# Kernel optimization log

Measured on AMD Instinct MI355X. Metric: run time of the kernel, lower is better.

## Reference

```python
import jax, jax.numpy as jnp
import numpy as np
from jax import lax

LEAK = 0.2
SCALE = 2.0 ** 0.5

def _make_blur_kernel(upsample_factor=1):
    k1 = jnp.array([1.0, 3.0, 3.0, 1.0], dtype=jnp.float32)
    k = k1[None, :] * k1[:, None]
    k = k / jnp.sum(k)
    return k * (upsample_factor ** 2)

def _modulate(weight, s):
    # weight [O,I,k,k], s [B,I] -> [B,O,I,k,k], demodulated
    wm = s[:, None, :, None, None] * weight[None]
    d = lax.rsqrt(jnp.sum(wm * wm, axis=(2, 3, 4)) + 1e-8)  # [B,O]
    return d[:, :, None, None, None] * wm

def _conv_transpose_sample(xi, wi):
    # xi [I,H,W], wi [O,I,k,k] (already ordered as wm[o,i]); torch conv_transpose2d(stride=2, pad=0)
    k = wi.shape[-1]
    y = lax.conv_general_dilated(xi[None], jnp.flip(wi, (-2, -1)), (1, 1),
                                 [(k - 1, k - 1), (k - 1, k - 1)], lhs_dilation=(2, 2),
                                 dimension_numbers=('NCHW', 'OIHW', 'NCHW'))
    return y[0]

def _conv_same_sample(xi, wi):
    y = lax.conv_general_dilated(xi[None], wi, (1, 1), [(1, 1), (1, 1)],
                                 dimension_numbers=('NCHW', 'OIHW', 'NCHW'))
    return y[0]

def _blur(x, kern, pad):
    # upfirdn2d with up=1, down=1, pad=(pad,pad): depthwise correlate with flipped kernel
    C = x.shape[1]
    w = jnp.tile(jnp.flip(kern, (0, 1))[None, None], (C, 1, 1, 1))
    return lax.conv_general_dilated(x, w, (1, 1), [(pad, pad), (pad, pad)],
                                    feature_group_count=C,
                                    dimension_numbers=('NCHW', 'OIHW', 'NCHW'))

def _flrelu(x, b):
    y = x + b.reshape(1, -1, 1, 1)
    return jnp.where(y >= 0, y, LEAK * y) * SCALE

def setup_inputs() -> dict:
    key = jax.random.key(0)
    ks = jax.random.split(key, 15)
    B, Cin, Cout, L, H = 8, 512, 256, 512, 64
    return {
        'x': jax.random.normal(ks[0], (B, Cin, H, H), jnp.float32),
        'w1': jax.random.normal(ks[1], (B, L), jnp.float32),
        'w2': jax.random.normal(ks[2], (B, L), jnp.float32),
        'noise1': jax.random.normal(ks[3], (B, 1, 2 * H, 2 * H), jnp.float32),
        'noise2': jax.random.normal(ks[4], (B, 1, 2 * H, 2 * H), jnp.float32),
        'weight1': jax.random.normal(ks[5], (Cout, Cin, 3, 3), jnp.float32) * 0.1,
        'aff1_w': jax.random.normal(ks[6], (Cin, L), jnp.float32) * 0.04,
        'aff1_b': jax.random.normal(ks[7], (Cin,), jnp.float32) * 0.1,
        'weight2': jax.random.normal(ks[8], (Cout, Cout, 3, 3), jnp.float32) * 0.1,
        'aff2_w': jax.random.normal(ks[9], (Cout, L), jnp.float32) * 0.04,
        'aff2_b': jax.random.normal(ks[10], (Cout,), jnp.float32) * 0.1,
        'ns1': jax.random.normal(ks[11], (1, 1, 1, 1), jnp.float32) * 0.1,
        'ns2': jax.random.normal(ks[12], (1, 1, 1, 1), jnp.float32) * 0.1,
        'b1': jax.random.normal(ks[13], (Cout,), jnp.float32) * 0.1,
        'b2': jax.random.normal(ks[14], (Cout,), jnp.float32) * 0.1,
    }

def reference(x, w1, w2, noise1, noise2, weight1, aff1_w, aff1_b,
              weight2, aff2_w, aff2_b, ns1, ns2, b1, b2):
    # conv1: modulated conv_transpose (upsample), blur, noise, fused leaky relu
    s1 = w1 @ aff1_w.T + aff1_b + 1.0          # [B, Cin]
    wm1 = _modulate(weight1, s1)               # [B, O, I, 3, 3]
    y = jax.vmap(_conv_transpose_sample)(x, wm1)  # [B, O, 129, 129]
    y = _blur(y, _make_blur_kernel(2), 1)      # [B, O, 128, 128]
    y = y + ns1 * noise1
    y = _flrelu(y, b1)
    # conv2: modulated same-padding conv, noise, fused leaky relu
    s2 = w2 @ aff2_w.T + aff2_b + 1.0
    wm2 = _modulate(weight2, s2)
    y = jax.vmap(_conv_same_sample)(y, wm2)
    y = y + ns2 * noise2
    y = _flrelu(y, b2)
    return y
```

## Files before the change

kernel.cpp:

```cpp
#include <hip/hip_runtime.h>
#include <hip/hip_bf16.h>

#define SQRT2C 1.41421356237309515f
#define LEAKF 0.2f

typedef __attribute__((ext_vector_type(4))) float f32x4;
typedef __attribute__((ext_vector_type(8))) __bf16 bf16x8;
typedef unsigned int u32x4 __attribute__((ext_vector_type(4)));

#define GLOAD16(g, l) \
  __builtin_amdgcn_global_load_lds((const __attribute__((address_space(1))) void*)(const void*)(g), \
                                   (__attribute__((address_space(3))) void*)(void*)(l), 16, 0, 0)

__device__ __forceinline__ unsigned short f2bf(float f) {
  unsigned int u = __float_as_uint(f);
  unsigned int r = (u + 0x7fffu + ((u >> 16) & 1u)) >> 16;
  return (unsigned short)r;
}
__device__ __forceinline__ float bflo(unsigned int w) { return __uint_as_float(w << 16); }
__device__ __forceinline__ float bfhi(unsigned int w) { return __uint_as_float(w & 0xffff0000u); }

constexpr float B1v(int c) { return (c < 0 || c > 3) ? 0.f : ((c == 0 || c == 3) ? 1.f : 3.f); }

__global__ void k_affine(const float* __restrict__ w, const float* __restrict__ aw,
                         const float* __restrict__ ab, float* __restrict__ s, int C) {
  int wid = (blockIdx.x * blockDim.x + threadIdx.x) >> 6;
  int lane = threadIdx.x & 63;
  int b = wid / C, i = wid % C;
  const float* wr = w + (size_t)b * 512;
  const float* ar = aw + (size_t)i * 512;
  float acc = 0.f;
  #pragma unroll
  for (int l = 0; l < 512; l += 64) acc += wr[l + lane] * ar[l + lane];
  #pragma unroll
  for (int off = 32; off; off >>= 1) acc += __shfl_down(acc, off, 64);
  if (lane == 0) s[wid] = acc + ab[i] + 1.0f;
}

__global__ void k_demod(const float* __restrict__ weight, const float* __restrict__ s,
                        float* __restrict__ d, int CIN) {
  int o = blockIdx.x & 255, b = blockIdx.x >> 8;
  int t = threadIdx.x;
  const float* wr = weight + (size_t)o * CIN * 9;
  const float* sr = s + (size_t)b * CIN;
  float acc = 0.f;
  for (int i = t; i < CIN; i += 256) {
    float sv = sr[i];
    float ws = 0.f;
    #pragma unroll
    for (int k = 0; k < 9; ++k) { float w = wr[(size_t)i * 9 + k]; ws += w * w; }
    acc += sv * sv * ws;
  }
  __shared__ float red[256];
  red[t] = acc; __syncthreads();
  for (int h = 128; h; h >>= 1) { if (t < h) red[t] += red[t + h]; __syncthreads(); }
  if (t == 0) d[blockIdx.x] = rsqrtf(red[0] + 1e-8f);
}

__global__ void k_wvert(const float* __restrict__ w1, const float* __restrict__ s1,
                        const float* __restrict__ d1, unsigned short* __restrict__ Wv) {
  int t = blockIdx.x * 256 + threadIdx.x;
  int i = t & 511, o = (t >> 9) & 255, b = t >> 17;
  float sd = s1[b * 512 + i] * d1[b * 256 + o];
  const float* wp = w1 + ((size_t)o * 512 + i) * 9;
  float wm[3][3];
  #pragma unroll
  for (int ky = 0; ky < 3; ++ky)
    #pragma unroll
    for (int kx = 0; kx < 3; ++kx) wm[ky][kx] = wp[ky * 3 + kx] * sd;
  #pragma unroll
  for (int rp = 0; rp < 2; ++rp)
    #pragma unroll
    for (int u = 0; u < 3; ++u)
      #pragma unroll
      for (int kx = 0; kx < 3; ++kx) {
        float v = 0.f;
        #pragma unroll
        for (int ky = 0; ky < 3; ++ky) v += B1v(4 - 2 * u - ky + rp) * wm[ky][kx];
        Wv[(((size_t)(b * 6 + rp * 3 + kx)) * 3 + u) * 131072 + (size_t)o * 512 + i] = f2bf(v);
      }
}

__global__ void k_weff2(const float* __restrict__ w2, const float* __restrict__ s2,
                        const float* __restrict__ d2, unsigned short* __restrict__ Wm) {
  int t = blockIdx.x * 256 + threadIdx.x;
  int i = t & 255, o = (t >> 8) & 255, b = t >> 16;
  float sd = s2[b * 256 + i] * d2[b * 256 + o];
  const float* wp = w2 + ((size_t)o * 256 + i) * 9;
  #pragma unroll
  for (int k = 0; k < 9; ++k)
    Wm[((size_t)(b * 9 + k) * 256 + o) * 256 + i] = f2bf(wp[k] * sd);
}

__global__ void k_border_y1(unsigned short* __restrict__ y1p) {
  int t = blockIdx.x * 256 + threadIdx.x;
  int l = t & 31;
  int c = (t >> 5) % 516;
  int b = (t >> 5) / 516;
  int p_, q_;
  if (c < 130)      { p_ = 0;       q_ = c; }
  else if (c < 260) { p_ = 129;     q_ = c - 130; }
  else if (c < 388) { p_ = c - 259; q_ = 0; }
  else              { p_ = c - 387; q_ = 129; }
  uint4* p = (uint4*)(y1p + (((size_t)(b * 130) + p_) * 130 + q_) * 256);
  p[l] = make_uint4(0u, 0u, 0u, 0u);
}

__global__ void k_fillv(unsigned short* __restrict__ xt) {
  int t = blockIdx.x * 256 + threadIdx.x;
  int j = t & 4095;
  int r = (t >> 12) & 1;
  int b = t >> 13;
  uint4* p = (uint4*)(xt + ((size_t)(b * 66) + (r ? 65 : 0)) * 64 * 512);
  p[j] = make_uint4(0u, 0u, 0u, 0u);
}

__global__ void k_txpose(const float* __restrict__ x, unsigned short* __restrict__ xt) {
  int bid = blockIdx.x;
  int i0 = (bid & 7) * 64;
  int x0 = ((bid >> 3) & 1) * 32;
  int y  = (bid >> 4) & 63;
  int b  = bid >> 10;
  int tx = threadIdx.x & 31, ty = threadIdx.x >> 5;
  __shared__ float tile[64][33];
  const float* xp = x + ((size_t)(b * 512 + i0) * 64 + y) * 64 + x0;
  for (int ii = ty; ii < 64; ii += 8) tile[ii][tx] = xp[(size_t)ii * 4096 + tx];
  __syncthreads();
  unsigned short* op = xt + (((size_t)(b * 66) + y + 1) * 64 + x0) * 512 + i0;
  for (int xx = ty; xx < 32; xx += 8) {
    int iL = tx * 2;
    unsigned int pk = (unsigned int)f2bf(tile[iL][xx]) | ((unsigned int)f2bf(tile[iL + 1][xx]) << 16);
    *(unsigned int*)&op[(size_t)xx * 512 + iL] = pk;
  }
}

template<int CIN, int GSH, int HP, int RHO_N, int TAPS, int PANB, int OM>
__global__ __launch_bounds__(512, 2) void k_conv8(
    const unsigned short* __restrict__ Xt,
    const unsigned short* __restrict__ Wt,
    const float* __restrict__ noise,
    const float* __restrict__ nsp,
    const float* __restrict__ bias,
    unsigned short* __restrict__ Yb,
    float* __restrict__ Yf)
{
  constexpr int GRID = 1 << GSH;
  constexpr int NT = (GRID * GRID) / 256;
  constexpr int NKT = TAPS * (CIN / 32);
  constexpr int KMASK = (CIN / 32) - 1;
  constexpr int KSH = (CIN == 512) ? 4 : 3;
  constexpr int TOT = NT * RHO_N * 8;
  constexpr int ROWW = (OM == 3) ? GRID : HP;
  extern __shared__ char smem[];

  int bid0 = blockIdx.x;
  int bid = (bid0 & 7) * (TOT / 8) + (bid0 >> 3);
  int nt = bid % NT;
  int rho = (bid / NT) % RHO_N;
  int b = bid / (NT * RHO_N);
  int pix0 = nt * 256;
  int tid = threadIdx.x, lane = tid & 63, w = tid >> 6;
  int lr = lane & 15, lq = lane >> 4;
  int wr = w >> 2, wc = w & 3;

  int p_ = lane & 7;
  int l8 = lane >> 3;
  int s0 = p_ ^ l8;
  int hs = s0 >> 2;
  int koffs = (s0 & 3) * 8;
  int rowA0 = 32 * w + 2 * l8 + hs;
  const unsigned short* Wp = Wt + ((size_t)b * PANB + rho * TAPS) * 256 * CIN;
  int aLane0 = rowA0 * CIN + koffs;
  int px0 = pix0 + 32 * w + 2 * l8 + hs;
  int gy0 = px0 >> GSH,        gx0 = px0 & (GRID - 1);
  int gy1 = (px0 + 16) >> GSH, gx1 = (px0 + 16) & (GRID - 1);
  const unsigned short* pB0 = Xt + (((size_t)b * HP + gy0) * ROWW + gx0) * CIN + koffs;
  const unsigned short* pB1 = Xt + (((size_t)b * HP + gy1) * ROWW + gx1) * CIN + koffs;
  int dstA = w * 2048;
  int dstB = 16384 + w * 2048;

  int xorterm = (((lr & 1) << 6) | (lq << 4)) ^ (((lr >> 1) & 7) << 4);
  int ldsAr = (wr * 64 + (lr >> 1)) * 128 + xorterm;
  int ldsBr = 16384 + (wc * 32 + (lr >> 1)) * 128 + xorterm;

  #pragma unroll
  for (int kt = 0; kt < 2; ++kt) {
    int ko = kt << 5;
    const unsigned short* sa = Wp + ko + aLane0;
    char* da = smem + (kt << 15) + dstA;
    GLOAD16(sa, da);
    GLOAD16(sa + 16 * CIN, da + 1024);
    char* db = smem + (kt << 15) + dstB;
    GLOAD16(pB0 + ko, db);
    GLOAD16(pB1 + ko, db + 1024);
  }
  asm volatile("s_waitcnt vmcnt(4)" ::: "memory");
  __builtin_amdgcn_s_barrier();

  f32x4 acc[8][4];
  #pragma unroll
  for (int m = 0; m < 8; ++m)
    #pragma unroll
    for (int n = 0; n < 4; ++n) acc[m][n] = (f32x4){0.f, 0.f, 0.f, 0.f};

  #pragma unroll 1
  for (int t = 0; t < NKT; ++t) {
    const char* Ab = smem + ((t & 3) << 15);
    bf16x8 bv[4], af[4];

    if (t + 2 < NKT) {
      int k2 = t + 2;
      int tap2 = k2 >> KSH, ko2 = (k2 & KMASK) << 5;
      const unsigned short* sa = Wp + (size_t)tap2 * (256 * CIN) + ko2 + aLane0;
      char* da = smem + ((k2 & 3) << 15) + dstA;
      GLOAD16(sa, da);
      GLOAD16(sa + 16 * CIN, da + 1024);
      size_t toff2 = (OM == 3) ? ((size_t)tap2 * GRID * CIN)
                               : (((size_t)(tap2 / 3) * HP + (tap2 % 3)) * CIN);
      char* db = smem + ((k2 & 3) << 15) + dstB;
      GLOAD16(pB0 + toff2 + ko2, db);
      GLOAD16(pB1 + toff2 + ko2, db + 1024);
    }

    #pragma unroll
    for (int n = 0; n < 4; ++n) bv[n] = *(const bf16x8*)(Ab + ldsBr + n * 1024);
    #pragma unroll
    for (int m = 0; m < 4; ++m) af[m] = *(const bf16x8*)(Ab + ldsAr + m * 1024);
    __builtin_amdgcn_s_setprio(1);
    #pragma unroll
    for (int m = 0; m < 4; ++m)
      #pragma unroll
      for (int n = 0; n < 4; ++n)
        acc[m][n] = __builtin_amdgcn_mfma_f32_16x16x32_bf16(af[m], bv[n], acc[m][n], 0, 0, 0);
    __builtin_amdgcn_s_setprio(0);
    #pragma unroll
    for (int m = 0; m < 4; ++m) af[m] = *(const bf16x8*)(Ab + ldsAr + (m + 4) * 1024);
    __builtin_amdgcn_s_setprio(1);
    #pragma unroll
    for (int m = 0; m < 4; ++m)
      #pragma unroll
      for (int n = 0; n < 4; ++n)
        acc[m + 4][n] = __builtin_amdgcn_mfma_f32_16x16x32_bf16(af[m], bv[n], acc[m + 4][n], 0, 0, 0);
    __builtin_amdgcn_s_setprio(0);

    if (t + 2 < NKT)      { asm volatile("s_waitcnt vmcnt(4)" ::: "memory"); }
    else if (t + 1 < NKT) { asm volatile("s_waitcnt vmcnt(0)" ::: "memory"); }
    __builtin_amdgcn_s_barrier();
  }

  if constexpr (OM == 2) {
    float ns = nsp[0];
    #pragma unroll
    for (int m = 0; m < 8; ++m) {
      int o = wr * 128 + m * 16 + lq * 4;
      #pragma unroll
      for (int n = 0; n < 4; ++n) {
        int pix = pix0 + wc * 64 + n * 16 + lr;
        int p = pix >> 7, q = pix & 127;
        float nz = ns * noise[((size_t)b << 14) + (p << 7) + q];
        #pragma unroll
        for (int r = 0; r < 4; ++r) {
          float v = acc[m][n][r] + nz + bias[o + r];
          v = (v >= 0.f ? v : LEAKF * v) * SQRT2C;
          __builtin_nontemporal_store(v, &Yf[(((size_t)b * 256 + o + r) << 14) + (p << 7) + q]);
        }
      }
    }
  } else {
    int rp = rho / 3, kx = rho % 3;
    #pragma unroll
    for (int m = 0; m < 8; ++m) {
      int o = wr * 128 + m * 16 + lq * 4;
      #pragma unroll
      for (int n = 0; n < 4; ++n) {
        int pix = pix0 + wc * 64 + n * 16 + lr;
        int p2 = ((pix >> 6) << 1) + rp, gxp = pix & 63;
        ushort4 pk;
        #pragma unroll
        for (int r = 0; r < 4; ++r) ((unsigned short*)&pk)[r] = f2bf(acc[m][n][r]);
        *(ushort4*)&Yb[((((size_t)(b * 3) + kx) * 128 + p2) * 64 + gxp) * 256 + o] = pk;
      }
    }
  }
}

__global__ void k_hmix(const unsigned short* __restrict__ A, const float* __restrict__ noise,
                       const float* __restrict__ nsp, const float* __restrict__ bias,
                       unsigned short* __restrict__ y1p) {
  int bid = blockIdx.x;
  int qg = bid & 15;
  int p = (bid >> 4) & 127;
  int b = bid >> 11;
  int o0 = (threadIdx.x & 31) * 8;
  int q = qg * 8 + (threadIdx.x >> 5);
  int gq = q >> 1;
  float rqf = (float)(q & 1);
  float acc[8];
  #pragma unroll
  for (int r = 0; r < 8; ++r) acc[r] = 0.f;
  #pragma unroll
  for (int v = 0; v < 3; ++v) {
    int gxx = gq + v - 1;
    float bmask = (gxx >= 0 && gxx <= 63) ? 1.f : 0.f;
    int gxc = gxx < 0 ? 0 : (gxx > 63 ? 63 : gxx);
    #pragma unroll
    for (int kx = 0; kx < 3; ++kx) {
      float C0 = B1v(4 - 2 * v - kx);
      float C1 = B1v(5 - 2 * v - kx);
      if (C0 == 0.f && C1 == 0.f) continue;
      float coef = (C0 + (C1 - C0) * rqf) * bmask;
      u32x4 av = __builtin_nontemporal_load(
          (const u32x4*)&A[(((size_t)(b * 3 + kx) * 128 + p) * 64 + gxc) * 256 + o0]);
      acc[0] += coef * bflo(av[0]); acc[1] += coef * bfhi(av[0]);
      acc[2] += coef * bflo(av[1]); acc[3] += coef * bfhi(av[1]);
      acc[4] += coef * bflo(av[2]); acc[5] += coef * bfhi(av[2]);
      acc[6] += coef * bflo(av[3]); acc[7] += coef * bfhi(av[3]);
    }
  }
  float ns = nsp[0];
  float nz = ns * noise[((size_t)b << 14) + (p << 7) + q];
  float4 bl = *(const float4*)&bias[o0];
  float4 bh = *(const float4*)&bias[o0 + 4];
  float bb[8] = {bl.x, bl.y, bl.z, bl.w, bh.x, bh.y, bh.z, bh.w};
  unsigned short ov[8];
  #pragma unroll
  for (int r = 0; r < 8; ++r) {
    float vv = acc[r] * 0.0625f + nz + bb[r];
    vv = (vv >= 0.f ? vv : LEAKF * vv) * SQRT2C;
    ov[r] = f2bf(vv);
  }
  uint4 pk;
  pk.x = (unsigned)ov[0] | ((unsigned)ov[1] << 16);
  pk.y = (unsigned)ov[2] | ((unsigned)ov[3] << 16);
  pk.z = (unsigned)ov[4] | ((unsigned)ov[5] << 16);
  pk.w = (unsigned)ov[6] | ((unsigned)ov[7] << 16);
  *(uint4*)&y1p[(((size_t)(b * 130) + p + 1) * 130 + q + 1) * 256 + o0] = pk;
}

extern "C" void kernel_launch(void* const* d_in, const int* in_sizes, int n_in,
                              void* d_out, int out_size, void* d_ws, size_t ws_size,
                              hipStream_t stream) {
  (void)in_sizes; (void)n_in; (void)out_size; (void)ws_size;
  const float* x       = (const float*)d_in[0];
  const float* w1      = (const float*)d_in[1];
  const float* w2      = (const float*)d_in[2];
  const float* noise1  = (const float*)d_in[3];
  const float* noise2  = (const float*)d_in[4];
  const float* weight1 = (const float*)d_in[5];
  const float* aff1w   = (const float*)d_in[6];
  const float* aff1b   = (const float*)d_in[7];
  const float* weight2 = (const float*)d_in[8];
  const float* aff2w   = (const float*)d_in[9];
  const float* aff2b   = (const float*)d_in[10];
  const float* ns1     = (const float*)d_in[11];
  const float* ns2     = (const float*)d_in[12];
  const float* b1      = (const float*)d_in[13];
  const float* b2      = (const float*)d_in[14];

  char* ws = (char*)d_ws;
  float* s1 = (float*)(ws + 0);
  float* s2 = (float*)(ws + 16384);
  float* d1 = (float*)(ws + 24576);
  float* d2 = (float*)(ws + 32768);
  unsigned short* xt   = (unsigned short*)(ws + 40960);
  unsigned short* Wv   = (unsigned short*)(ws + 34643968);
  unsigned short* W2m  = (unsigned short*)(ws + 72392704);
  unsigned short* A    = (unsigned short*)(ws + 81829888);
  unsigned short* y1p  = (unsigned short*)(ws + 40960);

  hipFuncSetAttribute((const void*)k_conv8<512, 6, 66, 6, 3, 18, 3>,
                      hipFuncAttributeMaxDynamicSharedMemorySize, 131072);
  hipFuncSetAttribute((const void*)k_conv8<256, 7, 130, 1, 9, 9, 2>,
                      hipFuncAttributeMaxDynamicSharedMemorySize, 131072);

  k_affine<<<1024, 256, 0, stream>>>(w1, aff1w, aff1b, s1, 512);
  k_affine<<<512,  256, 0, stream>>>(w2, aff2w, aff2b, s2, 256);
  k_demod<<<2048, 256, 0, stream>>>(weight1, s1, d1, 512);
  k_demod<<<2048, 256, 0, stream>>>(weight2, s2, d2, 256);
  k_wvert<<<4096, 256, 0, stream>>>(weight1, s1, d1, Wv);
  k_weff2<<<2048, 256, 0, stream>>>(weight2, s2, d2, W2m);
  k_fillv<<<256, 256, 0, stream>>>(xt);
  k_txpose<<<8192, 256, 0, stream>>>(x, xt);

  k_conv8<512, 6, 66, 6, 3, 18, 3><<<768, 512, 131072, stream>>>(
      xt, Wv, nullptr, nullptr, nullptr, A, nullptr);

  k_border_y1<<<516, 256, 0, stream>>>(y1p);
  k_hmix<<<16384, 256, 0, stream>>>(A, noise1, ns1, b1, y1p);
  k_conv8<256, 7, 130, 1, 9, 9, 2><<<512, 512, 131072, stream>>>(
      y1p, W2m, noise2, ns2, b2, nullptr, (float*)d_out);
}
```

Baseline: 414.3 us.

## Restructure implicit-GEMM main loop into 8-phase ping-pong pipeline with K=64 tiles

```diff
diff --git a/kernel.cpp b/kernel.cpp
--- a/kernel.cpp
+++ b/kernel.cpp
@@ -135,7 +135,7 @@
 }
 
 template<int CIN, int GSH, int HP, int RHO_N, int TAPS, int PANB, int OM>
-__global__ __launch_bounds__(512, 2) void k_conv8(
+__global__ __launch_bounds__(512, 2) void k_gemm8p(
     const unsigned short* __restrict__ Xt,
     const unsigned short* __restrict__ Wt,
     const float* __restrict__ noise,
@@ -146,11 +146,11 @@
 {
   constexpr int GRID = 1 << GSH;
   constexpr int NT = (GRID * GRID) / 256;
-  constexpr int NKT = TAPS * (CIN / 32);
-  constexpr int KMASK = (CIN / 32) - 1;
-  constexpr int KSH = (CIN == 512) ? 4 : 3;
+  constexpr int NKT = TAPS * (CIN / 64);
+  constexpr int NIT = NKT / 2;
+  constexpr int KSH = (CIN == 512) ? 3 : 2;
+  constexpr int KMASK = (CIN / 64) - 1;
   constexpr int TOT = NT * RHO_N * 8;
-  constexpr int ROWW = (OM == 3) ? GRID : HP;
   extern __shared__ char smem[];
 
   int bid0 = blockIdx.x;
@@ -162,91 +162,124 @@
   int tid = threadIdx.x, lane = tid & 63, w = tid >> 6;
   int lr = lane & 15, lq = lane >> 4;
   int wr = w >> 2, wc = w & 3;
-
-  int p_ = lane & 7;
-  int l8 = lane >> 3;
-  int s0 = p_ ^ l8;
-  int hs = s0 >> 2;
-  int koffs = (s0 & 3) * 8;
-  int rowA0 = 32 * w + 2 * l8 + hs;
+  int lhi = lane >> 3, llo = lane & 7;
+  int ksrc = ((llo ^ lhi) << 3);
+
   const unsigned short* Wp = Wt + ((size_t)b * PANB + rho * TAPS) * 256 * CIN;
-  int aLane0 = rowA0 * CIN + koffs;
-  int px0 = pix0 + 32 * w + 2 * l8 + hs;
-  int gy0 = px0 >> GSH,        gx0 = px0 & (GRID - 1);
-  int gy1 = (px0 + 16) >> GSH, gx1 = (px0 + 16) & (GRID - 1);
-  const unsigned short* pB0 = Xt + (((size_t)b * HP + gy0) * ROWW + gx0) * CIN + koffs;
-  const unsigned short* pB1 = Xt + (((size_t)b * HP + gy1) * ROWW + gx1) * CIN + koffs;
-  int dstA = w * 2048;
-  int dstB = 16384 + w * 2048;
-
-  int xorterm = (((lr & 1) << 6) | (lq << 4)) ^ (((lr >> 1) & 7) << 4);
-  int ldsAr = (wr * 64 + (lr >> 1)) * 128 + xorterm;
-  int ldsBr = 16384 + (wc * 32 + (lr >> 1)) * 128 + xorterm;
-
-  #pragma unroll
-  for (int kt = 0; kt < 2; ++kt) {
-    int ko = kt << 5;
-    const unsigned short* sa = Wp + ko + aLane0;
-    char* da = smem + (kt << 15) + dstA;
-    GLOAD16(sa, da);
-    GLOAD16(sa + 16 * CIN, da + 1024);
-    char* db = smem + (kt << 15) + dstB;
-    GLOAD16(pB0 + ko, db);
-    GLOAD16(pB1 + ko, db + 1024);
-  }
+  size_t aOff = (size_t)(w * 8 + lhi) * CIN + ksrc;
+  size_t bOff = (size_t)lhi * CIN + ksrc;
+  const unsigned short* XtB;
+  if constexpr (OM == 3) XtB = Xt + (size_t)b * HP * 64 * CIN;
+  else                   XtB = Xt + ((size_t)(b * HP + (pix0 >> 7))) * 130 * CIN;
+
+  auto stageA = [&](int buf, int t, int u) {
+    int tap = t >> KSH; size_t ke = (size_t)((t & KMASK) << 6);
+    const unsigned short* s = Wp + (size_t)tap * 256 * CIN + ke + (size_t)u * 64 * CIN + aOff;
+    char* d = smem + buf * 65536 + u * 8192 + w * 1024;
+    GLOAD16(s, d);
+    GLOAD16(s + (size_t)128 * CIN, d + 16384);
+  };
+  auto stageB = [&](int buf, int t, int u) {
+    int tap = t >> KSH; size_t ke = (size_t)((t & KMASK) << 6);
+    size_t tk;
+    if constexpr (OM == 3) tk = (size_t)tap * 64 * CIN + ke;
+    else                   tk = ((size_t)(tap / 3) * HP + (tap % 3)) * CIN + ke;
+    int c0 = w >> 2, r0 = (w & 3) * 8;
+    int rowA = c0 * 64 + u * 32 + r0;
+    int rowB = rowA + 128;
+    char* db = smem + buf * 65536 + 32768;
+    size_t sA, sB;
+    if constexpr (OM == 3) { sA = (size_t)(pix0 + rowA) * CIN; sB = (size_t)(pix0 + rowB) * CIN; }
+    else { sA = ((size_t)(rowA >> 7) * 130 + (rowA & 127)) * CIN;
+           sB = ((size_t)(rowB >> 7) * 130 + (rowB & 127)) * CIN; }
+    GLOAD16(XtB + sA + tk + bOff, db + rowA * 128);
+    GLOAD16(XtB + sB + tk + bOff, db + rowB * 128);
+  };
+
+  int ldsA = (wr * 128 + lr) * 128;
+  int ldsB = 32768 + (wc * 64 + lr) * 128;
+  int xk[2] = { (lq * 16) ^ ((lr & 7) << 4), (64 + lq * 16) ^ ((lr & 7) << 4) };
+
+  f32x4 acc[8][4];
+  #pragma unroll
+  for (int m = 0; m < 8; ++m)
+    #pragma unroll
+    for (int n = 0; n < 4; ++n) acc[m][n] = (f32x4){0.f, 0.f, 0.f, 0.f};
+
+  bf16x8 af[2][4], bv[2][4];
+  auto readA = [&](const char* base, int mq) {
+    #pragma unroll
+    for (int kk = 0; kk < 2; ++kk)
+      #pragma unroll
+      for (int m = 0; m < 4; ++m)
+        af[kk][m] = *(const bf16x8*)(base + ldsA + (mq * 4 + m) * 2048 + xk[kk]);
+  };
+  auto readB = [&](const char* base, int nq) {
+    #pragma unroll
+    for (int kk = 0; kk < 2; ++kk)
+      #pragma unroll
+      for (int n = 0; n < 2; ++n)
+        bv[kk][nq * 2 + n] = *(const bf16x8*)(base + ldsB + (nq * 2 + n) * 2048 + xk[kk]);
+  };
+  auto mma = [&](int mq, int nq) {
+    __builtin_amdgcn_s_setprio(1);
+    #pragma unroll
+    for (int kk = 0; kk < 2; ++kk)
+      #pragma unroll
+      for (int m = 0; m < 4; ++m)
+        #pragma unroll
+        for (int n = 0; n < 2; ++n)
+          acc[mq * 4 + m][nq * 2 + n] = __builtin_amdgcn_mfma_f32_16x16x32_bf16(
+              af[kk][m], bv[kk][nq * 2 + n], acc[mq * 4 + m][nq * 2 + n], 0, 0, 0);
+    __builtin_amdgcn_s_setprio(0);
+  };
+
+#define PH_SYNC()  __builtin_amdgcn_s_barrier(); \
+                   asm volatile("s_waitcnt lgkmcnt(0)" ::: "memory")
+#define PH_END()   __builtin_amdgcn_s_barrier()
+
+  stageA(0, 0, 0); stageB(0, 0, 0); stageA(0, 0, 1); stageB(0, 0, 1);
+  stageA(1, 1, 0); stageB(1, 1, 0);
   asm volatile("s_waitcnt vmcnt(4)" ::: "memory");
   __builtin_amdgcn_s_barrier();
 
-  f32x4 acc[8][4];
-  #pragma unroll
-  for (int m = 0; m < 8; ++m)
-    #pragma unroll
-    for (int n = 0; n < 4; ++n) acc[m][n] = (f32x4){0.f, 0.f, 0.f, 0.f};
+  const char* B0 = smem;
+  const char* B1 = smem + 65536;
 
   #pragma unroll 1
-  for (int t = 0; t < NKT; ++t) {
-    const char* Ab = smem + ((t & 3) << 15);
-    bf16x8 bv[4], af[4];
-
-    if (t + 2 < NKT) {
-      int k2 = t + 2;
-      int tap2 = k2 >> KSH, ko2 = (k2 & KMASK) << 5;
-      const unsigned short* sa = Wp + (size_t)tap2 * (256 * CIN) + ko2 + aLane0;
-      char* da = smem + ((k2 & 3) << 15) + dstA;
-      GLOAD16(sa, da);
-      GLOAD16(sa + 16 * CIN, da + 1024);
-      size_t toff2 = (OM == 3) ? ((size_t)tap2 * GRID * CIN)
-                               : (((size_t)(tap2 / 3) * HP + (tap2 % 3)) * CIN);
-      char* db = smem + ((k2 & 3) << 15) + dstB;
-      GLOAD16(pB0 + toff2 + ko2, db);
-      GLOAD16(pB1 + toff2 + ko2, db + 1024);
-    }
-
-    #pragma unroll
-    for (int n = 0; n < 4; ++n) bv[n] = *(const bf16x8*)(Ab + ldsBr + n * 1024);
-    #pragma unroll
-    for (int m = 0; m < 4; ++m) af[m] = *(const bf16x8*)(Ab + ldsAr + m * 1024);
-    __builtin_amdgcn_s_setprio(1);
-    #pragma unroll
-    for (int m = 0; m < 4; ++m)
-      #pragma unroll
-      for (int n = 0; n < 4; ++n)
-        acc[m][n] = __builtin_amdgcn_mfma_f32_16x16x32_bf16(af[m], bv[n], acc[m][n], 0, 0, 0);
-    __builtin_amdgcn_s_setprio(0);
-    #pragma unroll
-    for (int m = 0; m < 4; ++m) af[m] = *(const bf16x8*)(Ab + ldsAr + (m + 4) * 1024);
-    __builtin_amdgcn_s_setprio(1);
-    #pragma unroll
-    for (int m = 0; m < 4; ++m)
-      #pragma unroll
-      for (int n = 0; n < 4; ++n)
-        acc[m + 4][n] = __builtin_amdgcn_mfma_f32_16x16x32_bf16(af[m], bv[n], acc[m + 4][n], 0, 0, 0);
-    __builtin_amdgcn_s_setprio(0);
-
-    if (t + 2 < NKT)      { asm volatile("s_waitcnt vmcnt(4)" ::: "memory"); }
-    else if (t + 1 < NKT) { asm volatile("s_waitcnt vmcnt(0)" ::: "memory"); }
-    __builtin_amdgcn_s_barrier();
-  }
+  for (int i = 0; i < NIT; ++i) {
+    int a = 2 * i;
+    bool nl = (i + 1 < NIT);
+    readA(B0, 0); readB(B0, 0);
+    stageA(1, a + 1, 1);
+    PH_SYNC(); mma(0, 0); PH_END();
+    readB(B0, 1);
+    stageB(1, a + 1, 1);
+    PH_SYNC(); mma(0, 1); PH_END();
+    readA(B0, 1);
+    if (nl) stageA(0, a + 2, 0);
+    PH_SYNC(); mma(1, 0); PH_END();
+    if (nl) stageB(0, a + 2, 0);
+    PH_SYNC(); mma(1, 1);
+    if (nl) { asm volatile("s_waitcnt vmcnt(4)" ::: "memory"); }
+    else    { asm volatile("s_waitcnt vmcnt(0)" ::: "memory"); }
+    PH_END();
+    readA(B1, 0); readB(B1, 0);
+    if (nl) stageA(0, a + 2, 1);
+    PH_SYNC(); mma(0, 0); PH_END();
+    readB(B1, 1);
+    if (nl) stageB(0, a + 2, 1);
+    PH_SYNC(); mma(0, 1); PH_END();
+    readA(B1, 1);
+    if (nl) stageA(1, a + 3, 0);
+    PH_SYNC(); mma(1, 0); PH_END();
+    if (nl) stageB(1, a + 3, 0);
+    PH_SYNC(); mma(1, 1);
+    if (nl) { asm volatile("s_waitcnt vmcnt(4)" ::: "memory"); }
+    PH_END();
+  }
+#undef PH_SYNC
+#undef PH_END
 
   if constexpr (OM == 2) {
     float ns = nsp[0];
@@ -368,10 +401,10 @@
   unsigned short* A    = (unsigned short*)(ws + 81829888);
   unsigned short* y1p  = (unsigned short*)(ws + 40960);
 
-  hipFuncSetAttribute((const void*)k_conv8<512, 6, 66, 6, 3, 18, 3>,
-                      hipFuncAttributeMaxDynamicSharedMemorySize, 131072);
-  hipFuncSetAttribute((const void*)k_conv8<256, 7, 130, 1, 9, 9, 2>,
-                      hipFuncAttributeMaxDynamicSharedMemorySize, 131072);
+  (void)hipFuncSetAttribute((const void*)k_gemm8p<512, 6, 66, 6, 3, 18, 3>,
+                            hipFuncAttributeMaxDynamicSharedMemorySize, 131072);
+  (void)hipFuncSetAttribute((const void*)k_gemm8p<256, 7, 130, 1, 9, 9, 2>,
+                            hipFuncAttributeMaxDynamicSharedMemorySize, 131072);
 
   k_affine<<<1024, 256, 0, stream>>>(w1, aff1w, aff1b, s1, 512);
   k_affine<<<512,  256, 0, stream>>>(w2, aff2w, aff2b, s2, 256);
@@ -382,11 +415,11 @@
   k_fillv<<<256, 256, 0, stream>>>(xt);
   k_txpose<<<8192, 256, 0, stream>>>(x, xt);
 
-  k_conv8<512, 6, 66, 6, 3, 18, 3><<<768, 512, 131072, stream>>>(
+  k_gemm8p<512, 6, 66, 6, 3, 18, 3><<<768, 512, 131072, stream>>>(
       xt, Wv, nullptr, nullptr, nullptr, A, nullptr);
 
   k_border_y1<<<516, 256, 0, stream>>>(y1p);
   k_hmix<<<16384, 256, 0, stream>>>(A, noise1, ns1, b1, y1p);
-  k_conv8<256, 7, 130, 1, 9, 9, 2><<<512, 512, 131072, stream>>>(
+  k_gemm8p<256, 7, 130, 1, 9, 9, 2><<<512, 512, 131072, stream>>>(
       y1p, W2m, noise2, ns2, b2, nullptr, (float*)d_out);
 }
```

Result: faster. 399.5 us (-3.6%).
